# Performance work log

Hardware: AMD Instinct MI355X
Metric: run time of the kernel (lower is better)

The kernel has to match this reference:

```python
import jax, jax.numpy as jnp
import numpy as np

HIDDEN = 2048
N_EXPERTS = 64
TOP_K = 2
N_TOKENS = 16384


def setup_inputs() -> dict:
    key = jax.random.key(0)
    k1, k2 = jax.random.split(key)
    x = jax.random.normal(k1, (N_TOKENS, HIDDEN), dtype=jnp.float32)
    gate_w = jax.random.normal(k2, (N_EXPERTS, HIDDEN), dtype=jnp.float32) * (1.0 / np.sqrt(HIDDEN))
    gate_b = jnp.zeros((N_EXPERTS,), dtype=jnp.float32)
    return {"x": x, "gate_w": gate_w, "gate_b": gate_b}


def reference(x, gate_w, gate_b):
    # gate: [N, H] @ [H, E] + [E] -> [N, E]
    router_logits = jnp.einsum("nh,eh->ne", x, gate_w) + gate_b
    # softmax over experts in fp32 (matches F.softmax(..., dim=1, dtype=float32))
    router_probs = jax.nn.softmax(router_logits.astype(jnp.float32), axis=1)
    # top-k experts per token
    router_weights, selected_experts_indices = jax.lax.top_k(router_probs, TOP_K)  # [N, K]
    router_weights = router_weights / jnp.sum(router_weights, axis=-1, keepdims=True)
    router_weights = router_weights.astype(x.dtype)
    # one-hot [N, K, E] -> permute(2,1,0) -> [E, K, N]
    expert_mask = jax.nn.one_hot(selected_experts_indices, N_EXPERTS, dtype=jnp.int64 if jax.config.jax_enable_x64 else jnp.int32)
    expert_mask = jnp.transpose(expert_mask, (2, 1, 0))
    return (router_logits, router_weights, selected_experts_indices, expert_mask)
```

## Files before the change

kernel.cpp:

```cpp
#include <hip/hip_runtime.h>
#include <hip/hip_bf16.h>
#include <math.h>

#define HIDDEN 2048
#define NEXP   64
#define NTOK   16384
#define NTGF   256

typedef __attribute__((ext_vector_type(8))) _Float16 f16x8;
typedef __attribute__((ext_vector_type(4))) float   f32x4;

__device__ __forceinline__ void split2_f16(float4 f0, float4 f1, f16x8& h, f16x8& l) {
    float e[8] = {f0.x, f0.y, f0.z, f0.w, f1.x, f1.y, f1.z, f1.w};
    f16x8 hv, lv;
#pragma unroll
    for (int i = 0; i < 8; ++i) {
        _Float16 hh = (_Float16)e[i];
        float r = e[i] - (float)hh;
        hv[i] = hh;
        lv[i] = (_Float16)r;
    }
    h = hv; l = lv;
}

__global__ __launch_bounds__(256) void prep_kernel(
    const float* __restrict__ gw, uint4* __restrict__ wh, uint4* __restrict__ wl)
{
    const int gid = blockIdx.x * 256 + threadIdx.x;
    const int c   = gid >> 9;
    const int e   = (gid >> 3) & 63;
    const int kgp = gid & 7;
    const int kg  = kgp ^ (e & 7);
    const float* src = gw + (size_t)e * HIDDEN + c * 64 + kg * 8;
    float4 s0 = *(const float4*)src;
    float4 s1 = *(const float4*)(src + 4);
    f16x8 h, l;
    split2_f16(s0, s1, h, l);
    wh[gid] = __builtin_bit_cast(uint4, h);
    wl[gid] = __builtin_bit_cast(uint4, l);
}

#define STAGE(cg, bo)                                                                     \
    _Pragma("unroll")                                                                     \
    for (int rr = 0; rr < 2; ++rr) {                                                      \
        const int s = rr * 256 + tid;                                                     \
        __builtin_amdgcn_global_load_lds(                                                 \
            (const __attribute__((address_space(1))) void*)(wh + (size_t)(cg) * 512 + s), \
            (__attribute__((address_space(3))) void*)&Bs[(bo) + s], 16, 0, 0);            \
        __builtin_amdgcn_global_load_lds(                                                 \
            (const __attribute__((address_space(1))) void*)(wl + (size_t)(cg) * 512 + s), \
            (__attribute__((address_space(3))) void*)&Bs[(bo) + 512 + s], 16, 0, 0);      \
    }

__global__ __launch_bounds__(256, 2) void gemm_kernel(
    const float* __restrict__ x,
    const uint4* __restrict__ wh,
    const uint4* __restrict__ wl,
    float* __restrict__ part,
    int klen)
{
    __shared__ uint4 Bs[2 * 1024];

    const int tid = threadIdx.x;
    const int l   = tid & 63;
    const int wv  = tid >> 6;
    const int kg  = blockIdx.y;
    const int kbase = kg * klen;
    const int nch   = klen >> 6;
    const int cg0   = kbase >> 6;
    const int t0    = blockIdx.x * 128 + wv * 32;

    const float4* xp0 = (const float4*)(x + (size_t)(t0 + (l & 15)) * HIDDEN + kbase) + ((l >> 4) * 2);
    const float4* xp1 = (const float4*)(x + (size_t)(t0 + 16 + (l & 15)) * HIDDEN + kbase) + ((l >> 4) * 2);

    const int lb = ((l & 15) << 3) | ((l >> 4) ^ (l & 7));

    f32x4 acc1[2][4], acc2[2][4];
#pragma unroll
    for (int r = 0; r < 2; ++r)
#pragma unroll
        for (int eg = 0; eg < 4; ++eg) {
            acc1[r][eg] = (f32x4){0.f, 0.f, 0.f, 0.f};
            acc2[r][eg] = (f32x4){0.f, 0.f, 0.f, 0.f};
        }

    STAGE(cg0, 0)
    float4 a00 = xp0[0], a01 = xp0[1], a02 = xp0[8], a03 = xp0[9];
    float4 a10 = xp1[0], a11 = xp1[1], a12 = xp1[8], a13 = xp1[9];
    __syncthreads();

    for (int c = 0; c < nch; ++c) {
        const int buf = c & 1;
        float4 n00 = a00, n01 = a01, n02 = a02, n03 = a03;
        float4 n10 = a10, n11 = a11, n12 = a12, n13 = a13;
        if (c + 1 < nch) {
            STAGE(cg0 + c + 1, (buf ^ 1) * 1024)
            const int fb = (c + 1) * 16;
            n00 = xp0[fb + 0]; n01 = xp0[fb + 1]; n02 = xp0[fb + 8]; n03 = xp0[fb + 9];
            n10 = xp1[fb + 0]; n11 = xp1[fb + 1]; n12 = xp1[fb + 8]; n13 = xp1[fb + 9];
        }

#pragma unroll
        for (int ks = 0; ks < 2; ++ks) {
            f16x8 ah0, al0, ah1, al1;
            split2_f16(ks ? a02 : a00, ks ? a03 : a01, ah0, al0);
            split2_f16(ks ? a12 : a10, ks ? a13 : a11, ah1, al1);
            const int ib = buf * 1024 + (lb ^ (ks << 2));
#pragma unroll
            for (int eg = 0; eg < 4; ++eg) {
                f16x8 bh = __builtin_bit_cast(f16x8, Bs[ib + eg * 128]);
                f16x8 bl = __builtin_bit_cast(f16x8, Bs[ib + 512 + eg * 128]);
                acc1[0][eg] = __builtin_amdgcn_mfma_f32_16x16x32_f16(ah0, bh, acc1[0][eg], 0, 0, 0);
                acc2[0][eg] = __builtin_amdgcn_mfma_f32_16x16x32_f16(ah0, bl, acc2[0][eg], 0, 0, 0);
                acc2[0][eg] = __builtin_amdgcn_mfma_f32_16x16x32_f16(al0, bh, acc2[0][eg], 0, 0, 0);
                acc1[1][eg] = __builtin_amdgcn_mfma_f32_16x16x32_f16(ah1, bh, acc1[1][eg], 0, 0, 0);
                acc2[1][eg] = __builtin_amdgcn_mfma_f32_16x16x32_f16(ah1, bl, acc2[1][eg], 0, 0, 0);
                acc2[1][eg] = __builtin_amdgcn_mfma_f32_16x16x32_f16(al1, bh, acc2[1][eg], 0, 0, 0);
            }
        }
        a00 = n00; a01 = n01; a02 = n02; a03 = n03;
        a10 = n10; a11 = n11; a12 = n12; a13 = n13;
        __syncthreads();
    }

    float* pp = part + ((size_t)kg * NTOK + t0) * NEXP;
#pragma unroll
    for (int r = 0; r < 2; ++r)
#pragma unroll
        for (int eg = 0; eg < 4; ++eg)
#pragma unroll
            for (int i = 0; i < 4; ++i)
                pp[(size_t)(r * 16 + (l >> 4) * 4 + i) * NEXP + eg * 16 + (l & 15)] =
                    acc1[r][eg][i] + acc2[r][eg][i];
}

__global__ __launch_bounds__(256) void finish_kernel(
    const float* __restrict__ part,
    const float* __restrict__ bias_g,
    float* __restrict__ logits,
    float* __restrict__ weights,
    float* __restrict__ idxf,
    float* __restrict__ mask,
    int KS)
{
    __shared__ float Ls[64][65];
    __shared__ int selA[64], selB[64];

    const int tid = threadIdx.x;
    const int tg  = blockIdx.x;
    const int bm0 = tg * 64;
    const int tn  = tid & 15;
    const int tm  = tid >> 4;

    float4 acc[4];
#pragma unroll
    for (int i = 0; i < 4; ++i) acc[i] = make_float4(0.f, 0.f, 0.f, 0.f);

    for (int kg = 0; kg < KS; ++kg) {
        const float* pb = part + ((size_t)kg * NTOK + bm0) * NEXP;
#pragma unroll
        for (int i = 0; i < 4; ++i) {
            float4 v = *(const float4*)&pb[(4 * tm + i) * NEXP + 4 * tn];
            acc[i].x += v.x; acc[i].y += v.y; acc[i].z += v.z; acc[i].w += v.w;
        }
    }

    const float4 bv = *(const float4*)&bias_g[4 * tn];
#pragma unroll
    for (int i = 0; i < 4; ++i) {
        const int m = 4 * tm + i;
        float4 v;
        v.x = acc[i].x + bv.x;
        v.y = acc[i].y + bv.y;
        v.z = acc[i].z + bv.z;
        v.w = acc[i].w + bv.w;
        *(float4*)&logits[(size_t)(bm0 + m) * NEXP + 4 * tn] = v;
        Ls[m][4 * tn + 0] = v.x;
        Ls[m][4 * tn + 1] = v.y;
        Ls[m][4 * tn + 2] = v.z;
        Ls[m][4 * tn + 3] = v.w;
    }
    __syncthreads();

    if (tid < 64) {
        const int t = tid;
        float best = -1e30f, second = -1e30f;
        int bi = 0, si = 0;
#pragma unroll
        for (int e = 0; e < NEXP; ++e) {
            float v = Ls[t][e];
            if (v > best)        { second = best; si = bi; best = v; bi = e; }
            else if (v > second) { second = v; si = e; }
        }
        float r  = __expf(second - best);
        float w0 = 1.f / (1.f + r);
        float w1 = r / (1.f + r);
        const int tgl = bm0 + t;
        weights[2 * tgl + 0] = w0;
        weights[2 * tgl + 1] = w1;
        idxf[2 * tgl + 0] = (float)bi;
        idxf[2 * tgl + 1] = (float)si;
        selA[t] = bi;
        selB[t] = si;
    }
    __syncthreads();

    const int t4 = tid & 15;
    const int pg = tid >> 4;
    int sA0 = selA[4*t4+0], sA1 = selA[4*t4+1], sA2 = selA[4*t4+2], sA3 = selA[4*t4+3];
    int sB0 = selB[4*t4+0], sB1 = selB[4*t4+1], sB2 = selB[4*t4+2], sB3 = selB[4*t4+3];
#pragma unroll
    for (int p = 0; p < 8; ++p) {
        const int pair = pg * 8 + p;
        const int e = pair >> 1;
        const int k = pair & 1;
        const int a0 = k ? sB0 : sA0, a1 = k ? sB1 : sA1, a2 = k ? sB2 : sA2, a3 = k ? sB3 : sA3;
        float4 v;
        v.x = (a0 == e) ? 1.f : 0.f;
        v.y = (a1 == e) ? 1.f : 0.f;
        v.z = (a2 == e) ? 1.f : 0.f;
        v.w = (a3 == e) ? 1.f : 0.f;
        *(float4*)&mask[((size_t)e * 2 + k) * NTOK + bm0 + 4 * t4] = v;
    }
}

extern "C" void kernel_launch(void* const* d_in, const int* in_sizes, int n_in,
                              void* d_out, int out_size, void* d_ws, size_t ws_size,
                              hipStream_t stream) {
    const float* x  = (const float*)d_in[0];
    const float* gw = (const float*)d_in[1];
    const float* gb = (const float*)d_in[2];

    float* out     = (float*)d_out;
    float* logits  = out;
    float* weights = out + (size_t)NTOK * NEXP;
    float* idxf    = weights + (size_t)NTOK * 2;
    float* mask    = idxf + (size_t)NTOK * 2;

    uint4* wh = (uint4*)d_ws;
    uint4* wl = wh + 16384;
    const size_t hdrB   = 2 * 16384 * sizeof(uint4);
    const size_t sliceB = (size_t)NTOK * NEXP * sizeof(float);
    int KS;
    float* part;
    if      (ws_size >= hdrB + 4 * sliceB) { KS = 4; part = (float*)((char*)d_ws + hdrB); }
    else if (ws_size >= hdrB + 2 * sliceB) { KS = 2; part = (float*)((char*)d_ws + hdrB); }
    else                                   { KS = 1; part = logits; }

    const int klen = HIDDEN / KS;
    prep_kernel<<<64, 256, 0, stream>>>(gw, wh, wl);
    dim3 gridA(NTOK / 128, KS);
    gemm_kernel<<<gridA, 256, 0, stream>>>(x, wh, wl, part, klen);
    finish_kernel<<<NTGF, 256, 0, stream>>>(part, gb, logits, weights, idxf, mask, KS);
}
```

Baseline: 45.16 us.

## Fuse split-K reduction and routing epilogue into GEMM via last-block atomic fixup

Merges the split-K GEMM and the finish kernel into one launch. Each K-slice block bumps a per-tile atomic counter after writing its partials, and the last block to arrive reduces the four slices and does bias, top-2, weights and mask for its 128 tokens. The finish path now works on 32-token chunks, and the K length becomes a compile-time template parameter. This drops a kernel launch and the gap between kernels, at the cost of a serialized epilogue tail in the last-arriving blocks and extra shared memory per GEMM block.

```diff
diff --git a/kernel.cpp b/kernel.cpp
--- a/kernel.cpp
+++ b/kernel.cpp
@@ -5,7 +5,7 @@
 #define HIDDEN 2048
 #define NEXP   64
 #define NTOK   16384
-#define NTGF   256
+#define NTGF   512
 
 typedef __attribute__((ext_vector_type(8))) _Float16 f16x8;
 typedef __attribute__((ext_vector_type(4))) float   f32x4;
@@ -24,9 +24,11 @@
 }
 
 __global__ __launch_bounds__(256) void prep_kernel(
-    const float* __restrict__ gw, uint4* __restrict__ wh, uint4* __restrict__ wl)
+    const float* __restrict__ gw, uint4* __restrict__ wh, uint4* __restrict__ wl,
+    unsigned* __restrict__ cnt)
 {
     const int gid = blockIdx.x * 256 + threadIdx.x;
+    if (cnt && gid < 128) cnt[gid] = 0u;
     const int c   = gid >> 9;
     const int e   = (gid >> 3) & 63;
     const int kgp = gid & 7;
@@ -52,23 +54,17 @@
             (__attribute__((address_space(3))) void*)&Bs[(bo) + 512 + s], 16, 0, 0);      \
     }
 
-__global__ __launch_bounds__(256, 2) void gemm_kernel(
-    const float* __restrict__ x,
-    const uint4* __restrict__ wh,
-    const uint4* __restrict__ wl,
-    float* __restrict__ part,
-    int klen)
-{
-    __shared__ uint4 Bs[2 * 1024];
-
-    const int tid = threadIdx.x;
+template<int KLEN>
+__device__ __forceinline__ void gemm_body(
+    const float* __restrict__ x, const uint4* __restrict__ wh, const uint4* __restrict__ wl,
+    float* __restrict__ part, uint4* __restrict__ Bs, const int tid, const int bx, const int kg)
+{
     const int l   = tid & 63;
     const int wv  = tid >> 6;
-    const int kg  = blockIdx.y;
-    const int kbase = kg * klen;
-    const int nch   = klen >> 6;
+    const int kbase = kg * KLEN;
+    const int nch   = KLEN >> 6;
     const int cg0   = kbase >> 6;
-    const int t0    = blockIdx.x * 128 + wv * 32;
+    const int t0    = bx * 128 + wv * 32;
 
     const float4* xp0 = (const float4*)(x + (size_t)(t0 + (l & 15)) * HIDDEN + kbase) + ((l >> 4) * 2);
     const float4* xp1 = (const float4*)(x + (size_t)(t0 + 16 + (l & 15)) * HIDDEN + kbase) + ((l >> 4) * 2);
@@ -134,41 +130,32 @@
                     acc1[r][eg][i] + acc2[r][eg][i];
 }
 
-__global__ __launch_bounds__(256) void finish_kernel(
-    const float* __restrict__ part,
-    const float* __restrict__ bias_g,
-    float* __restrict__ logits,
-    float* __restrict__ weights,
-    float* __restrict__ idxf,
-    float* __restrict__ mask,
-    int KS)
-{
-    __shared__ float Ls[64][65];
-    __shared__ int selA[64], selB[64];
-
-    const int tid = threadIdx.x;
-    const int tg  = blockIdx.x;
-    const int bm0 = tg * 64;
-    const int tn  = tid & 15;
-    const int tm  = tid >> 4;
-
-    float4 acc[4];
-#pragma unroll
-    for (int i = 0; i < 4; ++i) acc[i] = make_float4(0.f, 0.f, 0.f, 0.f);
+__device__ __forceinline__ void finish_body(
+    const float* __restrict__ part, const float* __restrict__ bias_g,
+    float* __restrict__ logits, float* __restrict__ weights, float* __restrict__ idxf,
+    float* __restrict__ mask, const int KS, const int tid, const int bm0,
+    float (*Ls)[65], int* selA, int* selB)
+{
+    const int tn = tid & 15;
+    const int tm = tid >> 4;
+
+    float4 acc[2];
+#pragma unroll
+    for (int i = 0; i < 2; ++i) acc[i] = make_float4(0.f, 0.f, 0.f, 0.f);
 
     for (int kg = 0; kg < KS; ++kg) {
         const float* pb = part + ((size_t)kg * NTOK + bm0) * NEXP;
 #pragma unroll
-        for (int i = 0; i < 4; ++i) {
-            float4 v = *(const float4*)&pb[(4 * tm + i) * NEXP + 4 * tn];
+        for (int i = 0; i < 2; ++i) {
+            float4 v = *(const float4*)&pb[(tm + 16 * i) * NEXP + 4 * tn];
             acc[i].x += v.x; acc[i].y += v.y; acc[i].z += v.z; acc[i].w += v.w;
         }
     }
 
     const float4 bv = *(const float4*)&bias_g[4 * tn];
 #pragma unroll
-    for (int i = 0; i < 4; ++i) {
-        const int m = 4 * tm + i;
+    for (int i = 0; i < 2; ++i) {
+        const int m = tm + 16 * i;
         float4 v;
         v.x = acc[i].x + bv.x;
         v.y = acc[i].y + bv.y;
@@ -182,7 +169,7 @@
     }
     __syncthreads();
 
-    if (tid < 64) {
+    if (tid < 32) {
         const int t = tid;
         float best = -1e30f, second = -1e30f;
         int bi = 0, si = 0;
@@ -205,13 +192,14 @@
     }
     __syncthreads();
 
-    const int t4 = tid & 15;
-    const int pg = tid >> 4;
-    int sA0 = selA[4*t4+0], sA1 = selA[4*t4+1], sA2 = selA[4*t4+2], sA3 = selA[4*t4+3];
-    int sB0 = selB[4*t4+0], sB1 = selB[4*t4+1], sB2 = selB[4*t4+2], sB3 = selB[4*t4+3];
-#pragma unroll
-    for (int p = 0; p < 8; ++p) {
-        const int pair = pg * 8 + p;
+    const int t8 = tid & 7;
+    const int pg = tid >> 3;
+    const int b0 = 4 * t8;
+    int sA0 = selA[b0+0], sA1 = selA[b0+1], sA2 = selA[b0+2], sA3 = selA[b0+3];
+    int sB0 = selB[b0+0], sB1 = selB[b0+1], sB2 = selB[b0+2], sB3 = selB[b0+3];
+#pragma unroll
+    for (int p = 0; p < 4; ++p) {
+        const int pair = pg * 4 + p;
         const int e = pair >> 1;
         const int k = pair & 1;
         const int a0 = k ? sB0 : sA0, a1 = k ? sB1 : sA1, a2 = k ? sB2 : sA2, a3 = k ? sB3 : sA3;
@@ -220,8 +208,64 @@
         v.y = (a1 == e) ? 1.f : 0.f;
         v.z = (a2 == e) ? 1.f : 0.f;
         v.w = (a3 == e) ? 1.f : 0.f;
-        *(float4*)&mask[((size_t)e * 2 + k) * NTOK + bm0 + 4 * t4] = v;
-    }
+        *(float4*)&mask[((size_t)e * 2 + k) * NTOK + bm0 + b0] = v;
+    }
+}
+
+__global__ __launch_bounds__(256, 2) void gemm_fixup_kernel(
+    const float* __restrict__ x, const uint4* __restrict__ wh, const uint4* __restrict__ wl,
+    const float* __restrict__ bias_g, float* __restrict__ part, unsigned* __restrict__ cnt,
+    float* __restrict__ logits, float* __restrict__ weights, float* __restrict__ idxf,
+    float* __restrict__ mask)
+{
+    __shared__ uint4 Bs[2 * 1024];
+    __shared__ float Ls[32][65];
+    __shared__ int selA[32], selB[32];
+    __shared__ int lastFlag;
+
+    const int tid = threadIdx.x;
+    const int bx  = blockIdx.x;
+    const int kg  = blockIdx.y;
+
+    gemm_body<512>(x, wh, wl, part, Bs, tid, bx, kg);
+
+    __threadfence();
+    __syncthreads();
+    if (tid == 0) {
+        unsigned old = __hip_atomic_fetch_add(&cnt[bx], 1u, __ATOMIC_ACQ_REL,
+                                              __HIP_MEMORY_SCOPE_AGENT);
+        lastFlag = (old == 3u);
+    }
+    __syncthreads();
+
+    if (lastFlag) {
+        __threadfence();
+        for (int g = 0; g < 4; ++g) {
+            finish_body(part, bias_g, logits, weights, idxf, mask, 4, tid,
+                        bx * 128 + g * 32, Ls, selA, selB);
+            __syncthreads();
+        }
+    }
+}
+
+template<int KLEN>
+__global__ __launch_bounds__(256, 2) void gemm_kernel(
+    const float* __restrict__ x, const uint4* __restrict__ wh, const uint4* __restrict__ wl,
+    float* __restrict__ part)
+{
+    __shared__ uint4 Bs[2 * 1024];
+    gemm_body<KLEN>(x, wh, wl, part, Bs, threadIdx.x, blockIdx.x, blockIdx.y);
+}
+
+__global__ __launch_bounds__(256) void finish_kernel(
+    const float* __restrict__ part, const float* __restrict__ bias_g,
+    float* __restrict__ logits, float* __restrict__ weights, float* __restrict__ idxf,
+    float* __restrict__ mask, int KS)
+{
+    __shared__ float Ls[32][65];
+    __shared__ int selA[32], selB[32];
+    finish_body(part, bias_g, logits, weights, idxf, mask, KS, threadIdx.x, blockIdx.x * 32,
+                Ls, selA, selB);
 }
 
 extern "C" void kernel_launch(void* const* d_in, const int* in_sizes, int n_in,
@@ -241,15 +285,22 @@
     uint4* wl = wh + 16384;
     const size_t hdrB   = 2 * 16384 * sizeof(uint4);
     const size_t sliceB = (size_t)NTOK * NEXP * sizeof(float);
-    int KS;
-    float* part;
-    if      (ws_size >= hdrB + 4 * sliceB) { KS = 4; part = (float*)((char*)d_ws + hdrB); }
-    else if (ws_size >= hdrB + 2 * sliceB) { KS = 2; part = (float*)((char*)d_ws + hdrB); }
-    else                                   { KS = 1; part = logits; }
-
-    const int klen = HIDDEN / KS;
-    prep_kernel<<<64, 256, 0, stream>>>(gw, wh, wl);
-    dim3 gridA(NTOK / 128, KS);
-    gemm_kernel<<<gridA, 256, 0, stream>>>(x, wh, wl, part, klen);
-    finish_kernel<<<NTGF, 256, 0, stream>>>(part, gb, logits, weights, idxf, mask, KS);
-}
+    const size_t cntB   = 128 * sizeof(unsigned);
+
+    if (ws_size >= hdrB + 4 * sliceB + cntB) {
+        float*    part = (float*)((char*)d_ws + hdrB);
+        unsigned* cnt  = (unsigned*)((char*)d_ws + hdrB + 4 * sliceB);
+        prep_kernel<<<64, 256, 0, stream>>>(gw, wh, wl, cnt);
+        gemm_fixup_kernel<<<dim3(128, 4), 256, 0, stream>>>(
+            x, wh, wl, gb, part, cnt, logits, weights, idxf, mask);
+    } else if (ws_size >= hdrB + 4 * sliceB) {
+        float* part = (float*)((char*)d_ws + hdrB);
+        prep_kernel<<<64, 256, 0, stream>>>(gw, wh, wl, nullptr);
+        gemm_kernel<512><<<dim3(128, 4), 256, 0, stream>>>(x, wh, wl, part);
+        finish_kernel<<<NTGF, 256, 0, stream>>>(part, gb, logits, weights, idxf, mask, 4);
+    } else {
+        prep_kernel<<<64, 256, 0, stream>>>(gw, wh, wl, nullptr);
+        gemm_kernel<2048><<<dim3(128, 1), 256, 0, stream>>>(x, wh, wl, logits);
+        finish_kernel<<<NTGF, 256, 0, stream>>>(logits, gb, logits, weights, idxf, mask, 1);
+    }
+}
```

Result: slower. 143.6 us (+218.0%).
